# Optimization experiments

Measured on AMD Instinct MI355X. Metric: run time of the kernel, lower is better.

Reference implementation:

```python
import jax, jax.numpy as jnp
import numpy as np

NEG_SLOPE = 0.2

def gat_layer(x, W, al, ar, src, dst, n_dst):
    # x: [Ns, Fin]; W: [Fin, H*D]; al/ar: [H, D]; src/dst: [E]
    H, D = al.shape
    h = (x @ W).reshape(-1, H, D)          # [Ns, H, D]
    h_dst = h[:n_dst]                       # dst nodes are prefix of src nodes (DGL block)
    el = (h * al).sum(-1)                   # [Ns, H]
    er = (h_dst * ar).sum(-1)               # [Nd, H]
    e = jax.nn.leaky_relu(el[src] + er[dst], NEG_SLOPE)  # [E, H]
    m = jax.ops.segment_max(e, dst, num_segments=n_dst)  # stable edge-softmax
    a = jnp.exp(e - m[dst])
    s = jax.ops.segment_sum(a, dst, num_segments=n_dst)
    alpha = a / s[dst]                      # [E, H]
    msg = h[src] * alpha[:, :, None]        # [E, H, D]
    out = jax.ops.segment_sum(msg, dst, num_segments=n_dst)  # [Nd, H, D]
    return out.reshape(n_dst, H * D)


def setup_inputs() -> dict:
    key = jax.random.key(0)
    ks = jax.random.split(key, 16)
    N0, N1, N2, N3 = 200000, 100000, 50000, 25000
    E0, E1, E2 = 1000000, 500000, 250000
    Fin, Dh, H, C = 256, 64, 3, 40
    inp = {}
    inp['x'] = jax.random.normal(ks[0], (N0, Fin), jnp.float32)
    inp['src0'] = jax.random.randint(ks[1], (E0,), 0, N0, jnp.int32)
    inp['dst0'] = jnp.sort(jax.random.randint(ks[2], (E0,), 0, N1, jnp.int32))
    inp['src1'] = jax.random.randint(ks[3], (E1,), 0, N1, jnp.int32)
    inp['dst1'] = jnp.sort(jax.random.randint(ks[4], (E1,), 0, N2, jnp.int32))
    inp['src2'] = jax.random.randint(ks[5], (E2,), 0, N2, jnp.int32)
    inp['dst2'] = jnp.sort(jax.random.randint(ks[6], (E2,), 0, N3, jnp.int32))
    sc = lambda f: np.float32(1.0 / np.sqrt(f))
    inp['W0'] = jax.random.normal(ks[7], (Fin, H * Dh), jnp.float32) * sc(Fin)
    inp['al0'] = jax.random.normal(ks[8], (H, Dh), jnp.float32) * sc(Dh)
    inp['ar0'] = jax.random.normal(ks[9], (H, Dh), jnp.float32) * sc(Dh)
    inp['W1'] = jax.random.normal(ks[10], (H * Dh, H * Dh), jnp.float32) * sc(H * Dh)
    inp['al1'] = jax.random.normal(ks[11], (H, Dh), jnp.float32) * sc(Dh)
    inp['ar1'] = jax.random.normal(ks[12], (H, Dh), jnp.float32) * sc(Dh)
    inp['W2'] = jax.random.normal(ks[13], (H * Dh, C), jnp.float32) * sc(H * Dh)
    inp['al2'] = jax.random.normal(ks[14], (1, C), jnp.float32) * sc(C)
    inp['ar2'] = jax.random.normal(ks[15], (1, C), jnp.float32) * sc(C)
    return inp


def reference(x, src0, dst0, src1, dst1, src2, dst2,
              W0, al0, ar0, W1, al1, ar1, W2, al2, ar2):
    N1, N2, N3 = 100000, 50000, 25000
    h = gat_layer(x, W0, al0, ar0, src0, dst0, N1)
    h = jax.nn.relu(h)  # dropout is identity in eval/deterministic mode
    h = gat_layer(h, W1, al1, ar1, src1, dst1, N2)
    h = jax.nn.relu(h)
    out = gat_layer(h, W2, al2, ar2, src2, dst2, N3)  # [N3, n_classes]
    return out
```

## Files before the change

### kernel.cpp

```cpp
#include <hip/hip_runtime.h>
#include <math.h>

#define DEV_INLINE __device__ __forceinline__

typedef __attribute__((ext_vector_type(8))) short short8v;
typedef __attribute__((ext_vector_type(4))) float float4v;

DEV_INLINE unsigned short f2bf_rtn(float f) {
  unsigned u = __float_as_uint(f);
  u += 0x7FFFu + ((u >> 16) & 1u);
  return (unsigned short)(u >> 16);
}
DEV_INLINE float bf2f(unsigned short s) { return __uint_as_float(((unsigned)s) << 16); }

DEV_INLINE int soff(int row, int oct) { return row * 32 + ((oct ^ ((row >> 1) & 3)) << 3); }

DEV_INLINE void gload_lds16(const void* g, void* l) {
  __builtin_amdgcn_global_load_lds(
      (const __attribute__((address_space(1))) void*)g,
      (__attribute__((address_space(3))) void*)l, 16, 0, 0);
}

__global__ void conv_w_all(const float* __restrict__ W0, const float* __restrict__ W1,
                           const float* __restrict__ W2, short* __restrict__ w0h,
                           short* __restrict__ w0l, short* __restrict__ w1h,
                           short* __restrict__ w1l, short* __restrict__ w2h,
                           short* __restrict__ w2l) {
  const int S0 = 256 * 192, S1 = 192 * 192, S2 = 192 * 48;
  int idx = blockIdx.x * 256 + threadIdx.x;
  const float* W; short *Wh, *Wl; int K;
  int which;
  if (idx < S0) { W = W0; Wh = w0h; Wl = w0l; K = 256; which = 0; }
  else if (idx < S0 + S1) { idx -= S0; W = W1; Wh = w1h; Wl = w1l; K = 192; which = 1; }
  else if (idx < S0 + S1 + S2) { idx -= S0 + S1; W = W2; Wh = w2h; Wl = w2l; K = 192; which = 2; }
  else return;
  int n = idx / K, k = idx - n * K;
  if (which == 2 && n >= 40) { Wh[idx] = 0; Wl[idx] = 0; return; }
  int N = (which == 2) ? 40 : 192;
  float w = W[(size_t)k * N + n];
  unsigned short h = f2bf_rtn(w);
  Wh[idx] = (short)h;
  Wl[idx] = (short)f2bf_rtn(w - bf2f(h));
}

__global__ void csr_all(const int* __restrict__ d0, const int* __restrict__ d1,
                        const int* __restrict__ d2, int* __restrict__ o0,
                        int* __restrict__ o1, int* __restrict__ o2,
                        int E0, int E1, int E2, int n1, int n2, int n3) {
  int i = blockIdx.x * 256 + threadIdx.x;
  const int* dst; int* off; int E, nd;
  if (i < E0) { dst = d0; off = o0; E = E0; nd = n1; }
  else if (i < E0 + E1) { i -= E0; dst = d1; off = o1; E = E1; nd = n2; }
  else if (i < E0 + E1 + E2) { i -= E0 + E1; dst = d2; off = o2; E = E2; nd = n3; }
  else return;
  int d = dst[i];
  int p = (i == 0) ? -1 : dst[i - 1];
  for (int q = p + 1; q <= d; ++q) off[q] = i;
  if (i == E - 1)
    for (int q = d + 1; q <= nd; ++q) off[q] = E;
}

#define DMA_B(ktv, bufv)                                                      \
  {                                                                           \
    const int kb = (ktv) << 6;                                \
    for (int c = w; c < NT; c += 4) {                                         \
      gload_lds16((const char*)Bth + (size_t)c * (K * 32) + voff + kb,        \
                  (short*)Bs_h[bufv] + c * 512);                              \
      gload_lds16((const char*)Btl + (size_t)c * (K * 32) + voff + kb,        \
                  (short*)Bs_l[bufv] + c * 512);                              \
    }                                                                         \
  }

template <int NT, int H>
__global__ __launch_bounds__(256, 3) void gemm_fused(
    const float* __restrict__ A, const short* __restrict__ Bth,
    const short* __restrict__ Btl, const float* __restrict__ al,
    const float* __restrict__ ar, float* __restrict__ C,
    float* __restrict__ el, float* __restrict__ er,
    int M, int N, int K, int n_dst) {
  constexpr int BN = NT * 16;
  constexpr int TPH = NT / H;
  __shared__ short Bs_h[2][BN * 32], Bs_l[2][BN * 32];
  const int tid = threadIdx.x;
  const int w = tid >> 6, lane = tid & 63;
  const int quad = lane >> 4, l16 = lane & 15;
  const int m0 = blockIdx.x * 128;

  const int voff = (lane >> 2) * (K * 2) + ((((lane & 3) ^ ((lane >> 3) & 3))) << 4);

  float4v acc[2][NT];
#pragma unroll
  for (int mt = 0; mt < 2; ++mt)
#pragma unroll
    for (int nt = 0; nt < NT; ++nt)
#pragma unroll
      for (int r = 0; r < 4; ++r) acc[mt][nt][r] = 0.f;

  const int nk = K >> 5;
  DMA_B(0, 0);
  __syncthreads();

  for (int kt = 0; kt < nk; ++kt) {
    const int cur = kt & 1;
    float4 xa[2][2];
#pragma unroll
    for (int mt = 0; mt < 2; ++mt) {
      int row = m0 + w * 32 + mt * 16 + l16;
      if (row < M) {
        const float* ap = A + (size_t)row * K + (kt << 5) + quad * 8;
        xa[mt][0] = *(const float4*)ap;
        xa[mt][1] = *(const float4*)(ap + 4);
      } else {
        xa[mt][0] = make_float4(0.f, 0.f, 0.f, 0.f);
        xa[mt][1] = xa[mt][0];
      }
    }
    if (kt + 1 < nk) DMA_B(kt + 1, cur ^ 1);
    short8v afh[2], afl[2];
#pragma unroll
    for (int mt = 0; mt < 2; ++mt) {
      float vs[8] = {xa[mt][0].x, xa[mt][0].y, xa[mt][0].z, xa[mt][0].w,
                     xa[mt][1].x, xa[mt][1].y, xa[mt][1].z, xa[mt][1].w};
#pragma unroll
      for (int j = 0; j < 8; ++j) {
        unsigned short hh = f2bf_rtn(vs[j]);
        afh[mt][j] = (short)hh;
        afl[mt][j] = (short)f2bf_rtn(vs[j] - bf2f(hh));
      }
    }
#pragma unroll
    for (int nt = 0; nt < NT; ++nt) {
      int col = nt * 16 + l16;
      short8v bfh = *(const short8v*)(Bs_h[cur] + soff(col, quad));
      short8v bfl = *(const short8v*)(Bs_l[cur] + soff(col, quad));
#pragma unroll
      for (int mt = 0; mt < 2; ++mt) {
        acc[mt][nt] = __builtin_amdgcn_mfma_f32_16x16x32_bf16(afh[mt], bfh, acc[mt][nt], 0, 0, 0);
        acc[mt][nt] = __builtin_amdgcn_mfma_f32_16x16x32_bf16(afh[mt], bfl, acc[mt][nt], 0, 0, 0);
        acc[mt][nt] = __builtin_amdgcn_mfma_f32_16x16x32_bf16(afl[mt], bfh, acc[mt][nt], 0, 0, 0);
      }
    }
    if (kt + 1 < nk) __syncthreads();
  }

  float av[NT], rv[NT];
#pragma unroll
  for (int nt = 0; nt < NT; ++nt) {
    int col = nt * 16 + l16;
    av[nt] = (col < N) ? al[col] : 0.f;
    rv[nt] = (col < N) ? ar[col] : 0.f;
  }
#pragma unroll
  for (int mt = 0; mt < 2; ++mt)
#pragma unroll
    for (int r = 0; r < 4; ++r) {
      int gm = m0 + w * 32 + mt * 16 + quad * 4 + r;
      if (gm >= M) continue;
      float pl[H], pr[H];
#pragma unroll
      for (int h = 0; h < H; ++h) { pl[h] = 0.f; pr[h] = 0.f; }
#pragma unroll
      for (int nt = 0; nt < NT; ++nt) {
        int h = nt / TPH;
        pl[h] = fmaf(acc[mt][nt][r], av[nt], pl[h]);
        pr[h] = fmaf(acc[mt][nt][r], rv[nt], pr[h]);
      }
#pragma unroll
      for (int h = 0; h < H; ++h) {
#pragma unroll
        for (int o = 8; o >= 1; o >>= 1) {
          pl[h] += __shfl_xor(pl[h], o, 16);
          pr[h] += __shfl_xor(pr[h], o, 16);
        }
      }
      if (l16 == 0) {
#pragma unroll
        for (int h = 0; h < H; ++h) {
          el[gm * H + h] = pl[h];
          if (gm < n_dst) er[gm * H + h] = pr[h];
        }
      }
#pragma unroll
      for (int nt = 0; nt < NT; ++nt) {
        int col = nt * 16 + l16;
        if (col < N) C[(size_t)gm * N + col] = acc[mt][nt][r];
      }
    }
}

template <int H, int D, bool RELU>
__global__ __launch_bounds__(256) void agg2_kernel(
    const float* __restrict__ hsrc, const float* __restrict__ el,
    const float* __restrict__ er, const int* __restrict__ src,
    const int* __restrict__ off, float* __restrict__ out, int n_dst) {
  constexpr int F = H * D;
  constexpr int NP = (F + 63) / 64;
  __shared__ float wbuf[16][16][H];
  __shared__ int sbuf[16][16];
  const int g = threadIdx.x >> 4, l = threadIdx.x & 15;
  const int d = blockIdx.x * 16 + g;
  if (d >= n_dst) return;
  const int lo = off[d], hi = off[d + 1];

  if (hi <= lo) {
#pragma unroll
    for (int p = 0; p < NP; ++p) {
      int c4 = (p * 16 + l) * 4;
      if (c4 < F) *(float4*)(out + (size_t)d * F + c4) = make_float4(0.f, 0.f, 0.f, 0.f);
    }
    return;
  }

  float erv[H], s_part[H];
#pragma unroll
  for (int h = 0; h < H; ++h) {
    erv[h] = er[d * H + h];
    s_part[h] = 0.f;
  }
  float4 acc[NP];
#pragma unroll
  for (int p = 0; p < NP; ++p) acc[p] = make_float4(0.f, 0.f, 0.f, 0.f);

  for (int base = lo; base < hi; base += 16) {
    const int i = base + l;
    const bool valid = i < hi;
    const int sid = valid ? src[i] : 0;
#pragma unroll
    for (int h = 0; h < H; ++h) {
      float e = 0.f;
      if (valid) {
        e = el[sid * H + h] + erv[h];
        e = e > 0.f ? e : 0.2f * e;
        e = __expf(e);
      }
      s_part[h] += e;
      wbuf[g][l][h] = e;
    }
    sbuf[g][l] = sid;

    const int cnt = min(16, hi - base);
    int sj = sbuf[g][0];
    float4 hv[NP], hn[NP];
#pragma unroll
    for (int p = 0; p < NP; ++p) {
      int c4 = (p * 16 + l) * 4;
      hv[p] = (c4 < F) ? *(const float4*)(hsrc + (size_t)sj * F + c4)
                       : make_float4(0.f, 0.f, 0.f, 0.f);
    }
    for (int ei = 0; ei < cnt; ++ei) {
      if (ei + 1 < cnt) {
        int sj2 = sbuf[g][ei + 1];
#pragma unroll
        for (int p = 0; p < NP; ++p) {
          int c4 = (p * 16 + l) * 4;
          hn[p] = (c4 < F) ? *(const float4*)(hsrc + (size_t)sj2 * F + c4)
                           : make_float4(0.f, 0.f, 0.f, 0.f);
        }
      }
#pragma unroll
      for (int p = 0; p < NP; ++p) {
        int c4 = (p * 16 + l) * 4;
        float wc = wbuf[g][ei][c4 / D];
        acc[p].x = fmaf(wc, hv[p].x, acc[p].x);
        acc[p].y = fmaf(wc, hv[p].y, acc[p].y);
        acc[p].z = fmaf(wc, hv[p].z, acc[p].z);
        acc[p].w = fmaf(wc, hv[p].w, acc[p].w);
      }
#pragma unroll
      for (int p = 0; p < NP; ++p) hv[p] = hn[p];
    }
  }

#pragma unroll
  for (int h = 0; h < H; ++h)
#pragma unroll
    for (int o = 8; o >= 1; o >>= 1) s_part[h] += __shfl_xor(s_part[h], o, 16);

#pragma unroll
  for (int p = 0; p < NP; ++p) {
    int c4 = (p * 16 + l) * 4;
    if (c4 < F) {
      float inv = 1.f / s_part[c4 / D];
      float4 o;
      o.x = acc[p].x * inv; o.y = acc[p].y * inv;
      o.z = acc[p].z * inv; o.w = acc[p].w * inv;
      if (RELU) {
        o.x = fmaxf(o.x, 0.f); o.y = fmaxf(o.y, 0.f);
        o.z = fmaxf(o.z, 0.f); o.w = fmaxf(o.w, 0.f);
      }
      *(float4*)(out + (size_t)d * F + c4) = o;
    }
  }
}

extern "C" void kernel_launch(void* const* d_in, const int* in_sizes, int n_in,
                              void* d_out, int out_size, void* d_ws, size_t ws_size,
                              hipStream_t stream) {
  const float* x   = (const float*)d_in[0];
  const int* src0  = (const int*)d_in[1];
  const int* dst0  = (const int*)d_in[2];
  const int* src1  = (const int*)d_in[3];
  const int* dst1  = (const int*)d_in[4];
  const int* src2  = (const int*)d_in[5];
  const int* dst2  = (const int*)d_in[6];
  const float* W0  = (const float*)d_in[7];
  const float* al0 = (const float*)d_in[8];
  const float* ar0 = (const float*)d_in[9];
  const float* W1  = (const float*)d_in[10];
  const float* al1 = (const float*)d_in[11];
  const float* ar1 = (const float*)d_in[12];
  const float* W2  = (const float*)d_in[13];
  const float* al2 = (const float*)d_in[14];
  const float* ar2 = (const float*)d_in[15];

  const int N0 = 200000, N1 = 100000, N2 = 50000, N3 = 25000;
  const int E0 = in_sizes[1], E1 = in_sizes[3], E2 = in_sizes[5];
  const int Fin = 256, F = 192, C = 40;

  float* ws     = (float*)d_ws;
  float* h_buf  = ws;
  float* o_buf  = h_buf + (size_t)N0 * F;
  float* el_buf = o_buf + (size_t)N1 * F;
  float* er_buf = el_buf + (size_t)N0 * 3;
  short* w0h    = (short*)(er_buf + (size_t)N1 * 3);
  short* w0l    = w0h + 192 * 256;
  short* w1h    = w0l + 192 * 256;
  short* w1l    = w1h + 192 * 192;
  short* w2h    = w1l + 192 * 192;
  short* w2l    = w2h + 48 * 192;
  int*   off0   = (int*)(w2l + 48 * 192);
  int*   off1   = off0 + (N1 + 1);
  int*   off2   = off1 + (N2 + 1);

  dim3 blk(256);

  const int WTOT = 256 * 192 + 192 * 192 + 192 * 48;
  conv_w_all<<<dim3((WTOT + 255) / 256), blk, 0, stream>>>(W0, W1, W2, w0h, w0l, w1h, w1l, w2h, w2l);
  const int ETOT = E0 + E1 + E2;
  csr_all<<<dim3((ETOT + 255) / 256), blk, 0, stream>>>(dst0, dst1, dst2, off0, off1, off2,
                                                        E0, E1, E2, N1, N2, N3);

  gemm_fused<12, 3><<<dim3((N0 + 127) / 128), blk, 0, stream>>>(
      x, w0h, w0l, al0, ar0, h_buf, el_buf, er_buf, N0, F, Fin, N1);
  agg2_kernel<3, 64, true><<<dim3((N1 + 15) / 16), blk, 0, stream>>>(
      h_buf, el_buf, er_buf, src0, off0, o_buf, N1);

  gemm_fused<12, 3><<<dim3((N1 + 127) / 128), blk, 0, stream>>>(
      o_buf, w1h, w1l, al1, ar1, h_buf, el_buf, er_buf, N1, F, F, N2);
  agg2_kernel<3, 64, true><<<dim3((N2 + 15) / 16), blk, 0, stream>>>(
      h_buf, el_buf, er_buf, src1, off1, o_buf, N2);

  gemm_fused<3, 1><<<dim3((N2 + 127) / 128), blk, 0, stream>>>(
      o_buf, w2h, w2l, al2, ar2, h_buf, el_buf, er_buf, N2, C, F, N3);
  agg2_kernel<1, 40, false><<<dim3((N3 + 15) / 16), blk, 0, stream>>>(
      h_buf, el_buf, er_buf, src2, off2, (float*)d_out, N3);
}
```

Measured before the change: 637.8 us.

## Halve GEMM row tile, prefetch A one step ahead, deepen gather prefetch, merge prepass kernels

```diff
diff --git a/kernel.cpp b/kernel.cpp
--- a/kernel.cpp
+++ b/kernel.cpp
@@ -21,33 +21,34 @@
       (__attribute__((address_space(3))) void*)l, 16, 0, 0);
 }
 
-__global__ void conv_w_all(const float* __restrict__ W0, const float* __restrict__ W1,
-                           const float* __restrict__ W2, short* __restrict__ w0h,
-                           short* __restrict__ w0l, short* __restrict__ w1h,
-                           short* __restrict__ w1l, short* __restrict__ w2h,
-                           short* __restrict__ w2l) {
+__global__ void prepass_all(const float* __restrict__ W0, const float* __restrict__ W1,
+                            const float* __restrict__ W2, short* __restrict__ w0h,
+                            short* __restrict__ w0l, short* __restrict__ w1h,
+                            short* __restrict__ w1l, short* __restrict__ w2h,
+                            short* __restrict__ w2l,
+                            const int* __restrict__ d0, const int* __restrict__ d1,
+                            const int* __restrict__ d2, int* __restrict__ o0,
+                            int* __restrict__ o1, int* __restrict__ o2,
+                            int E0, int E1, int E2, int n1, int n2, int n3) {
   const int S0 = 256 * 192, S1 = 192 * 192, S2 = 192 * 48;
-  int idx = blockIdx.x * 256 + threadIdx.x;
-  const float* W; short *Wh, *Wl; int K;
-  int which;
-  if (idx < S0) { W = W0; Wh = w0h; Wl = w0l; K = 256; which = 0; }
-  else if (idx < S0 + S1) { idx -= S0; W = W1; Wh = w1h; Wl = w1l; K = 192; which = 1; }
-  else if (idx < S0 + S1 + S2) { idx -= S0 + S1; W = W2; Wh = w2h; Wl = w2l; K = 192; which = 2; }
-  else return;
-  int n = idx / K, k = idx - n * K;
-  if (which == 2 && n >= 40) { Wh[idx] = 0; Wl[idx] = 0; return; }
-  int N = (which == 2) ? 40 : 192;
-  float w = W[(size_t)k * N + n];
-  unsigned short h = f2bf_rtn(w);
-  Wh[idx] = (short)h;
-  Wl[idx] = (short)f2bf_rtn(w - bf2f(h));
-}
-
-__global__ void csr_all(const int* __restrict__ d0, const int* __restrict__ d1,
-                        const int* __restrict__ d2, int* __restrict__ o0,
-                        int* __restrict__ o1, int* __restrict__ o2,
-                        int E0, int E1, int E2, int n1, int n2, int n3) {
-  int i = blockIdx.x * 256 + threadIdx.x;
+  const int WTOT = S0 + S1 + S2;
+  int gidx = blockIdx.x * 256 + threadIdx.x;
+  if (gidx < WTOT) {
+    int idx = gidx;
+    const float* W; short *Wh, *Wl; int K; int which;
+    if (idx < S0) { W = W0; Wh = w0h; Wl = w0l; K = 256; which = 0; }
+    else if (idx < S0 + S1) { idx -= S0; W = W1; Wh = w1h; Wl = w1l; K = 192; which = 1; }
+    else { idx -= S0 + S1; W = W2; Wh = w2h; Wl = w2l; K = 192; which = 2; }
+    int n = idx / K, k = idx - n * K;
+    if (which == 2 && n >= 40) { Wh[idx] = 0; Wl[idx] = 0; return; }
+    int N = (which == 2) ? 40 : 192;
+    float w = W[(size_t)k * N + n];
+    unsigned short h = f2bf_rtn(w);
+    Wh[idx] = (short)h;
+    Wl[idx] = (short)f2bf_rtn(w - bf2f(h));
+    return;
+  }
+  int i = gidx - WTOT;
   const int* dst; int* off; int E, nd;
   if (i < E0) { dst = d0; off = o0; E = E0; nd = n1; }
   else if (i < E0 + E1) { i -= E0; dst = d1; off = o1; E = E1; nd = n2; }
@@ -84,48 +85,56 @@
   const int tid = threadIdx.x;
   const int w = tid >> 6, lane = tid & 63;
   const int quad = lane >> 4, l16 = lane & 15;
-  const int m0 = blockIdx.x * 128;
+  const int m0 = blockIdx.x * 64;
+  const int arow = m0 + w * 16 + l16;
 
   const int voff = (lane >> 2) * (K * 2) + ((((lane & 3) ^ ((lane >> 3) & 3))) << 4);
 
-  float4v acc[2][NT];
-#pragma unroll
-  for (int mt = 0; mt < 2; ++mt)
-#pragma unroll
-    for (int nt = 0; nt < NT; ++nt)
-#pragma unroll
-      for (int r = 0; r < 4; ++r) acc[mt][nt][r] = 0.f;
+  float4v acc[NT];
+#pragma unroll
+  for (int nt = 0; nt < NT; ++nt)
+#pragma unroll
+    for (int r = 0; r < 4; ++r) acc[nt][r] = 0.f;
 
   const int nk = K >> 5;
+
   DMA_B(0, 0);
+  float4 pa0, pa1;
+  if (arow < M) {
+    const float* ap = A + (size_t)arow * K + quad * 8;
+    pa0 = *(const float4*)ap;
+    pa1 = *(const float4*)(ap + 4);
+  } else {
+    pa0 = make_float4(0.f, 0.f, 0.f, 0.f);
+    pa1 = pa0;
+  }
   __syncthreads();
 
   for (int kt = 0; kt < nk; ++kt) {
     const int cur = kt & 1;
-    float4 xa[2][2];
-#pragma unroll
-    for (int mt = 0; mt < 2; ++mt) {
-      int row = m0 + w * 32 + mt * 16 + l16;
-      if (row < M) {
-        const float* ap = A + (size_t)row * K + (kt << 5) + quad * 8;
-        xa[mt][0] = *(const float4*)ap;
-        xa[mt][1] = *(const float4*)(ap + 4);
+    float4 na0, na1;
+    if (kt + 1 < nk) {
+      if (arow < M) {
+        const float* ap = A + (size_t)arow * K + ((kt + 1) << 5) + quad * 8;
+        na0 = *(const float4*)ap;
+        na1 = *(const float4*)(ap + 4);
       } else {
-        xa[mt][0] = make_float4(0.f, 0.f, 0.f, 0.f);
-        xa[mt][1] = xa[mt][0];
-      }
-    }
-    if (kt + 1 < nk) DMA_B(kt + 1, cur ^ 1);
-    short8v afh[2], afl[2];
-#pragma unroll
-    for (int mt = 0; mt < 2; ++mt) {
-      float vs[8] = {xa[mt][0].x, xa[mt][0].y, xa[mt][0].z, xa[mt][0].w,
-                     xa[mt][1].x, xa[mt][1].y, xa[mt][1].z, xa[mt][1].w};
+        na0 = make_float4(0.f, 0.f, 0.f, 0.f);
+        na1 = na0;
+      }
+      DMA_B(kt + 1, cur ^ 1);
+    } else {
+      na0 = make_float4(0.f, 0.f, 0.f, 0.f);
+      na1 = na0;
+    }
+    short8v afh, afl;
+    {
+      float vs[8] = {pa0.x, pa0.y, pa0.z, pa0.w, pa1.x, pa1.y, pa1.z, pa1.w};
 #pragma unroll
       for (int j = 0; j < 8; ++j) {
         unsigned short hh = f2bf_rtn(vs[j]);
-        afh[mt][j] = (short)hh;
-        afl[mt][j] = (short)f2bf_rtn(vs[j] - bf2f(hh));
+        afh[j] = (short)hh;
+        afl[j] = (short)f2bf_rtn(vs[j] - bf2f(hh));
       }
     }
 #pragma unroll
@@ -133,14 +142,13 @@
       int col = nt * 16 + l16;
       short8v bfh = *(const short8v*)(Bs_h[cur] + soff(col, quad));
       short8v bfl = *(const short8v*)(Bs_l[cur] + soff(col, quad));
-#pragma unroll
-      for (int mt = 0; mt < 2; ++mt) {
-        acc[mt][nt] = __builtin_amdgcn_mfma_f32_16x16x32_bf16(afh[mt], bfh, acc[mt][nt], 0, 0, 0);
-        acc[mt][nt] = __builtin_amdgcn_mfma_f32_16x16x32_bf16(afh[mt], bfl, acc[mt][nt], 0, 0, 0);
-        acc[mt][nt] = __builtin_amdgcn_mfma_f32_16x16x32_bf16(afl[mt], bfh, acc[mt][nt], 0, 0, 0);
-      }
+      acc[nt] = __builtin_amdgcn_mfma_f32_16x16x32_bf16(afh, bfh, acc[nt], 0, 0, 0);
+      acc[nt] = __builtin_amdgcn_mfma_f32_16x16x32_bf16(afh, bfl, acc[nt], 0, 0, 0);
+      acc[nt] = __builtin_amdgcn_mfma_f32_16x16x32_bf16(afl, bfh, acc[nt], 0, 0, 0);
     }
     if (kt + 1 < nk) __syncthreads();
+    pa0 = na0;
+    pa1 = na1;
   }
 
   float av[NT], rv[NT];
@@ -151,41 +159,39 @@
     rv[nt] = (col < N) ? ar[col] : 0.f;
   }
 #pragma unroll
-  for (int mt = 0; mt < 2; ++mt)
-#pragma unroll
-    for (int r = 0; r < 4; ++r) {
-      int gm = m0 + w * 32 + mt * 16 + quad * 4 + r;
-      if (gm >= M) continue;
-      float pl[H], pr[H];
-#pragma unroll
-      for (int h = 0; h < H; ++h) { pl[h] = 0.f; pr[h] = 0.f; }
-#pragma unroll
-      for (int nt = 0; nt < NT; ++nt) {
-        int h = nt / TPH;
-        pl[h] = fmaf(acc[mt][nt][r], av[nt], pl[h]);
-        pr[h] = fmaf(acc[mt][nt][r], rv[nt], pr[h]);
-      }
+  for (int r = 0; r < 4; ++r) {
+    int gm = m0 + w * 16 + quad * 4 + r;
+    if (gm >= M) continue;
+    float pl[H], pr[H];
+#pragma unroll
+    for (int h = 0; h < H; ++h) { pl[h] = 0.f; pr[h] = 0.f; }
+#pragma unroll
+    for (int nt = 0; nt < NT; ++nt) {
+      int h = nt / TPH;
+      pl[h] = fmaf(acc[nt][r], av[nt], pl[h]);
+      pr[h] = fmaf(acc[nt][r], rv[nt], pr[h]);
+    }
+#pragma unroll
+    for (int h = 0; h < H; ++h) {
+#pragma unroll
+      for (int o = 8; o >= 1; o >>= 1) {
+        pl[h] += __shfl_xor(pl[h], o, 16);
+        pr[h] += __shfl_xor(pr[h], o, 16);
+      }
+    }
+    if (l16 == 0) {
 #pragma unroll
       for (int h = 0; h < H; ++h) {
-#pragma unroll
-        for (int o = 8; o >= 1; o >>= 1) {
-          pl[h] += __shfl_xor(pl[h], o, 16);
-          pr[h] += __shfl_xor(pr[h], o, 16);
-        }
-      }
-      if (l16 == 0) {
-#pragma unroll
-        for (int h = 0; h < H; ++h) {
-          el[gm * H + h] = pl[h];
-          if (gm < n_dst) er[gm * H + h] = pr[h];
-        }
-      }
-#pragma unroll
-      for (int nt = 0; nt < NT; ++nt) {
-        int col = nt * 16 + l16;
-        if (col < N) C[(size_t)gm * N + col] = acc[mt][nt][r];
-      }
-    }
+        el[gm * H + h] = pl[h];
+        if (gm < n_dst) er[gm * H + h] = pr[h];
+      }
+    }
+#pragma unroll
+    for (int nt = 0; nt < NT; ++nt) {
+      int col = nt * 16 + l16;
+      if (col < N) C[(size_t)gm * N + col] = acc[nt][r];
+    }
+  }
 }
 
 template <int H, int D, bool RELU>
@@ -239,22 +245,33 @@
     sbuf[g][l] = sid;
 
     const int cnt = min(16, hi - base);
-    int sj = sbuf[g][0];
-    float4 hv[NP], hn[NP];
-#pragma unroll
-    for (int p = 0; p < NP; ++p) {
-      int c4 = (p * 16 + l) * 4;
-      hv[p] = (c4 < F) ? *(const float4*)(hsrc + (size_t)sj * F + c4)
-                       : make_float4(0.f, 0.f, 0.f, 0.f);
+    float4 hv[NP], hn[NP], hn2[NP];
+    {
+      int sj = sbuf[g][0];
+#pragma unroll
+      for (int p = 0; p < NP; ++p) {
+        int c4 = (p * 16 + l) * 4;
+        hv[p] = (c4 < F) ? *(const float4*)(hsrc + (size_t)sj * F + c4)
+                         : make_float4(0.f, 0.f, 0.f, 0.f);
+      }
+    }
+    if (cnt > 1) {
+      int sj = sbuf[g][1];
+#pragma unroll
+      for (int p = 0; p < NP; ++p) {
+        int c4 = (p * 16 + l) * 4;
+        hn[p] = (c4 < F) ? *(const float4*)(hsrc + (size_t)sj * F + c4)
+                         : make_float4(0.f, 0.f, 0.f, 0.f);
+      }
     }
     for (int ei = 0; ei < cnt; ++ei) {
-      if (ei + 1 < cnt) {
-        int sj2 = sbuf[g][ei + 1];
+      if (ei + 2 < cnt) {
+        int sj2 = sbuf[g][ei + 2];
 #pragma unroll
         for (int p = 0; p < NP; ++p) {
           int c4 = (p * 16 + l) * 4;
-          hn[p] = (c4 < F) ? *(const float4*)(hsrc + (size_t)sj2 * F + c4)
-                           : make_float4(0.f, 0.f, 0.f, 0.f);
+          hn2[p] = (c4 < F) ? *(const float4*)(hsrc + (size_t)sj2 * F + c4)
+                            : make_float4(0.f, 0.f, 0.f, 0.f);
         }
       }
 #pragma unroll
@@ -267,7 +284,7 @@
         acc[p].w = fmaf(wc, hv[p].w, acc[p].w);
       }
 #pragma unroll
-      for (int p = 0; p < NP; ++p) hv[p] = hn[p];
+      for (int p = 0; p < NP; ++p) { hv[p] = hn[p]; hn[p] = hn2[p]; }
     }
   }
 
@@ -335,22 +352,22 @@
   dim3 blk(256);
 
   const int WTOT = 256 * 192 + 192 * 192 + 192 * 48;
-  conv_w_all<<<dim3((WTOT + 255) / 256), blk, 0, stream>>>(W0, W1, W2, w0h, w0l, w1h, w1l, w2h, w2l);
   const int ETOT = E0 + E1 + E2;
-  csr_all<<<dim3((ETOT + 255) / 256), blk, 0, stream>>>(dst0, dst1, dst2, off0, off1, off2,
-                                                        E0, E1, E2, N1, N2, N3);
-
-  gemm_fused<12, 3><<<dim3((N0 + 127) / 128), blk, 0, stream>>>(
+  prepass_all<<<dim3((WTOT + ETOT + 255) / 256), blk, 0, stream>>>(
+      W0, W1, W2, w0h, w0l, w1h, w1l, w2h, w2l,
+      dst0, dst1, dst2, off0, off1, off2, E0, E1, E2, N1, N2, N3);
+
+  gemm_fused<12, 3><<<dim3((N0 + 63) / 64), blk, 0, stream>>>(
       x, w0h, w0l, al0, ar0, h_buf, el_buf, er_buf, N0, F, Fin, N1);
   agg2_kernel<3, 64, true><<<dim3((N1 + 15) / 16), blk, 0, stream>>>(
       h_buf, el_buf, er_buf, src0, off0, o_buf, N1);
 
-  gemm_fused<12, 3><<<dim3((N1 + 127) / 128), blk, 0, stream>>>(
+  gemm_fused<12, 3><<<dim3((N1 + 63) / 64), blk, 0, stream>>>(
       o_buf, w1h, w1l, al1, ar1, h_buf, el_buf, er_buf, N1, F, F, N2);
   agg2_kernel<3, 64, true><<<dim3((N2 + 15) / 16), blk, 0, stream>>>(
       h_buf, el_buf, er_buf, src1, off1, o_buf, N2);
 
-  gemm_fused<3, 1><<<dim3((N2 + 127) / 128), blk, 0, stream>>>(
+  gemm_fused<3, 1><<<dim3((N2 + 63) / 64), blk, 0, stream>>>(
       o_buf, w2h, w2l, al2, ar2, h_buf, el_buf, er_buf, N2, C, F, N3);
   agg2_kernel<1, 40, false><<<dim3((N3 + 15) / 16), blk, 0, stream>>>(
       h_buf, el_buf, er_buf, src2, off2, (float*)d_out, N3);
```

New measurement: 641.6 us. No clear change (+0.6%).
